# Kernel tuning notes

Hardware: AMD Instinct MI355X
Metric: run time of the kernel (lower is better)

Reference implementation:

```python
import jax, jax.numpy as jnp
import numpy as np

B = 8388608  # batch

def moth(x, a, b):
    # per-feature parametric elementwise activation: a * x * sigmoid(b * x)
    return a * x * jax.nn.sigmoid(b * x)

def setup_inputs() -> dict:
    key = jax.random.key(0)
    ks = jax.random.split(key, 12)
    inp = {
        'x':  jax.random.normal(ks[0], (B, 2), dtype=jnp.float32),
        'W1': jax.random.normal(ks[1], (2, 8), dtype=jnp.float32) * (1.0 / np.sqrt(2)),
        'b1': jax.random.normal(ks[2], (8,), dtype=jnp.float32) * 0.01,
        'a1': jax.random.normal(ks[3], (8,), dtype=jnp.float32) * 0.1 + 1.0,
        'c1': jax.random.normal(ks[4], (8,), dtype=jnp.float32) * 0.1 + 1.0,
        'W2': jax.random.normal(ks[5], (8, 4), dtype=jnp.float32) * (1.0 / np.sqrt(8)),
        'b2': jax.random.normal(ks[6], (4,), dtype=jnp.float32) * 0.01,
        'a2': jax.random.normal(ks[7], (4,), dtype=jnp.float32) * 0.1 + 1.0,
        'c2': jax.random.normal(ks[8], (4,), dtype=jnp.float32) * 0.1 + 1.0,
        'W3': jax.random.normal(ks[9], (4, 1), dtype=jnp.float32) * (1.0 / np.sqrt(4)),
        'b3': jax.random.normal(ks[10], (1,), dtype=jnp.float32) * 0.01,
    }
    return inp

def reference(x, W1, b1, a1, c1, W2, b2, a2, c2, W3, b3):
    h = x @ W1 + b1            # [B, 8]
    h = moth(h, a1, c1)        # [B, 8]
    h = h @ W2 + b2            # [B, 4]
    h = moth(h, a2, c2)        # [B, 4]
    out = h @ W3 + b3          # [B, 1]
    return out
```

## Files before the change

kernel.cpp:

```cpp
#include <hip/hip_runtime.h>

#define NLOG2E -1.44269504088896340736f

typedef float f32x2 __attribute__((ext_vector_type(2)));


__global__ void prefold_kernel(
    const float* __restrict__ W1, const float* __restrict__ b1,
    const float* __restrict__ a1, const float* __restrict__ c1,
    const float* __restrict__ W2, const float* __restrict__ b2,
    const float* __restrict__ a2, const float* __restrict__ c2,
    const float* __restrict__ W3, const float* __restrict__ b3,
    float* __restrict__ C)
{
    if (threadIdx.x == 0 && blockIdx.x == 0) {
        for (int j = 0; j < 8; ++j) {
            float ncl = c1[j] * NLOG2E;
            C[j]      = W1[j]     * ncl;
            C[8 + j]  = W1[8 + j] * ncl;
            C[16 + j] = b1[j]     * ncl;
            float k1 = a1[j] / ncl;
            for (int k = 0; k < 4; ++k)
                C[24 + j * 4 + k] = W2[j * 4 + k] * k1;
        }
        for (int k = 0; k < 4; ++k) {
            C[56 + k] = b2[k];
            C[60 + k] = c2[k] * NLOG2E;
            C[64 + k] = a2[k] * W3[k];
        }
        C[68] = b3[0];
    }
}

__device__ __forceinline__ f32x2 moth2(float4 p, const f32x2* __restrict__ Cp,
                                       float bb3)
{
    f32x2 u[2][4];
#pragma unroll
    for (int r = 0; r < 2; ++r) {
        float X0 = r ? p.z : p.x;
        float X1 = r ? p.w : p.y;
        f32x2 x0b = {X0, X0};
        f32x2 x1b = {X1, X1};
#pragma unroll
        for (int pj = 0; pj < 4; ++pj)
            u[r][pj] = __builtin_elementwise_fma(
                           x0b, Cp[pj],
                           __builtin_elementwise_fma(x1b, Cp[4 + pj],
                                                     Cp[8 + pj]));
    }

#pragma unroll
    for (int r = 0; r < 2; ++r)
#pragma unroll
        for (int pj = 0; pj < 4; ++pj) {
            f32x2 e;
            e[0] = __builtin_amdgcn_exp2f(u[r][pj][0]);
            e[1] = __builtin_amdgcn_exp2f(u[r][pj][1]);
            f32x2 d = e + 1.0f;
            f32x2 s;
            s[0] = __builtin_amdgcn_rcpf(d[0]);
            s[1] = __builtin_amdgcn_rcpf(d[1]);
            u[r][pj] *= s;
        }

    f32x2 res;
#pragma unroll
    for (int r = 0; r < 2; ++r) {
        f32x2 ta = Cp[28], tb = Cp[29];
#pragma unroll
        for (int j = 0; j < 8; ++j) {
            float hj = u[r][j >> 1][j & 1];
            f32x2 hb = {hj, hj};
            ta = __builtin_elementwise_fma(hb, Cp[12 + j * 2 + 0], ta);
            tb = __builtin_elementwise_fma(hb, Cp[12 + j * 2 + 1], tb);
        }
        f32x2 u2a = Cp[30] * ta;
        f32x2 u2b = Cp[31] * tb;
        f32x2 ea, eb;
        ea[0] = __builtin_amdgcn_exp2f(u2a[0]);
        ea[1] = __builtin_amdgcn_exp2f(u2a[1]);
        eb[0] = __builtin_amdgcn_exp2f(u2b[0]);
        eb[1] = __builtin_amdgcn_exp2f(u2b[1]);
        f32x2 da = ea + 1.0f, db = eb + 1.0f;
        f32x2 sa, sb;
        sa[0] = __builtin_amdgcn_rcpf(da[0]);
        sa[1] = __builtin_amdgcn_rcpf(da[1]);
        sb[0] = __builtin_amdgcn_rcpf(db[0]);
        sb[1] = __builtin_amdgcn_rcpf(db[1]);
        f32x2 pa = ta * sa;
        f32x2 pb = tb * sb;
        f32x2 acc = {bb3, 0.0f};
        acc = __builtin_elementwise_fma(pa, Cp[32], acc);
        acc = __builtin_elementwise_fma(pb, Cp[33], acc);
        res[r] = acc[0] + acc[1];
    }
    return res;
}

__global__ __launch_bounds__(256, 4) void PlaygroundModel_66365834658304_kernel(
    const float* __restrict__ x, const float* __restrict__ C,
    float* __restrict__ out, int rows)
{
    const f32x2* Cp = (const f32x2*)C;
    float bb3 = C[68];

    int g = blockIdx.x * blockDim.x + threadIdx.x;
    int lane = g & 63;
    long long idx0 = (long long)(g >> 6) * 256 + lane;
    long long n4f  = (long long)rows >> 1;

    const float4* x4 = (const float4*)x;
    f32x2* o2 = (f32x2*)out;

    if (idx0 + 192 < n4f) {
        float4 P0 = x4[idx0];
        float4 P1 = x4[idx0 + 64];
        float4 P2 = x4[idx0 + 128];
        float4 P3 = x4[idx0 + 192];
        o2[idx0]       = moth2(P0, Cp, bb3);
        o2[idx0 + 64]  = moth2(P1, Cp, bb3);
        o2[idx0 + 128] = moth2(P2, Cp, bb3);
        o2[idx0 + 192] = moth2(P3, Cp, bb3);
    } else {
        const float* uw0  = C;
        const float* uw1  = C + 8;
        const float* ub   = C + 16;
        const float* w2f  = C + 24;
        const float* bb2  = C + 56;
        const float* ncl2 = C + 60;
        const float* aw2  = C + 64;
#pragma unroll
        for (int k = 0; k < 4; ++k) {
            long long idx = idx0 + 64 * k;
            long long r0 = idx * 2;
            for (long long rr = r0; rr < r0 + 2 && rr < rows; ++rr) {
                float x0 = x[rr * 2 + 0], x1 = x[rr * 2 + 1];
                float h[8];
#pragma unroll
                for (int j = 0; j < 8; ++j) {
                    float uu = fmaf(x0, uw0[j], fmaf(x1, uw1[j], ub[j]));
                    float s  = __builtin_amdgcn_rcpf(
                                   1.0f + __builtin_amdgcn_exp2f(uu));
                    h[j] = uu * s;
                }
                float o = bb3;
#pragma unroll
                for (int kk = 0; kk < 4; ++kk) {
                    float t = bb2[kk];
#pragma unroll
                    for (int j = 0; j < 8; ++j)
                        t = fmaf(h[j], w2f[j * 4 + kk], t);
                    float u2 = ncl2[kk] * t;
                    float sg = __builtin_amdgcn_rcpf(
                                   1.0f + __builtin_amdgcn_exp2f(u2));
                    o = fmaf(t * sg, aw2[kk], o);
                }
                out[rr] = o;
            }
        }
    }
}

extern "C" void kernel_launch(void* const* d_in, const int* in_sizes, int n_in,
                              void* d_out, int out_size, void* d_ws, size_t ws_size,
                              hipStream_t stream) {
    const float* x  = (const float*)d_in[0];
    const float* W1 = (const float*)d_in[1];
    const float* b1 = (const float*)d_in[2];
    const float* a1 = (const float*)d_in[3];
    const float* c1 = (const float*)d_in[4];
    const float* W2 = (const float*)d_in[5];
    const float* b2 = (const float*)d_in[6];
    const float* a2 = (const float*)d_in[7];
    const float* c2 = (const float*)d_in[8];
    const float* W3 = (const float*)d_in[9];
    const float* b3 = (const float*)d_in[10];
    float* out = (float*)d_out;
    float* C   = (float*)d_ws;

    prefold_kernel<<<1, 64, 0, stream>>>(W1, b1, a1, c1, W2, b2, a2, c2,
                                         W3, b3, C);

    int rows = in_sizes[0] / 2;
    long long n4    = ((long long)rows + 1) / 2;
    long long waves = (n4 + 255) / 256;
    long long thr   = waves * 64;
    int block = 256;
    long long grid = (thr + block - 1) / block;
    if (grid < 1) grid = 1;

    PlaygroundModel_66365834658304_kernel<<<(int)grid, block, 0, stream>>>(
        x, C, out, rows);
}
```

Before: 127.1 us.

## Switch to grid-stride loop with software-prefetched loads and capped grid

```diff
diff --git a/kernel.cpp b/kernel.cpp
--- a/kernel.cpp
+++ b/kernel.cpp
@@ -98,31 +98,36 @@
     return res;
 }
 
-__global__ __launch_bounds__(256, 4) void PlaygroundModel_66365834658304_kernel(
+__global__ __launch_bounds__(256, 6) void PlaygroundModel_66365834658304_kernel(
     const float* __restrict__ x, const float* __restrict__ C,
     float* __restrict__ out, int rows)
 {
     const f32x2* Cp = (const f32x2*)C;
     float bb3 = C[68];
 
-    int g = blockIdx.x * blockDim.x + threadIdx.x;
-    int lane = g & 63;
-    long long idx0 = (long long)(g >> 6) * 256 + lane;
-    long long n4f  = (long long)rows >> 1;
+    long long n4f    = (long long)rows >> 1;
+    long long g      = (long long)blockIdx.x * blockDim.x + threadIdx.x;
+    long long stride = (long long)gridDim.x * blockDim.x;
 
     const float4* x4 = (const float4*)x;
     f32x2* o2 = (f32x2*)out;
 
-    if (idx0 + 192 < n4f) {
-        float4 P0 = x4[idx0];
-        float4 P1 = x4[idx0 + 64];
-        float4 P2 = x4[idx0 + 128];
-        float4 P3 = x4[idx0 + 192];
-        o2[idx0]       = moth2(P0, Cp, bb3);
-        o2[idx0 + 64]  = moth2(P1, Cp, bb3);
-        o2[idx0 + 128] = moth2(P2, Cp, bb3);
-        o2[idx0 + 192] = moth2(P3, Cp, bb3);
-    } else {
+    long long idx = g;
+    if (idx < n4f) {
+        float4 p = x4[idx];
+        for (;;) {
+            long long nidx = idx + stride;
+            bool has = (nidx < n4f);
+            float4 np;
+            if (has) np = x4[nidx];
+            o2[idx] = moth2(p, Cp, bb3);
+            if (!has) break;
+            p = np;
+            idx = nidx;
+        }
+    }
+
+    if (g == 0 && (rows & 1)) {
         const float* uw0  = C;
         const float* uw1  = C + 8;
         const float* ub   = C + 16;
@@ -130,35 +135,28 @@
         const float* bb2  = C + 56;
         const float* ncl2 = C + 60;
         const float* aw2  = C + 64;
+        long long rr = (long long)rows - 1;
+        float x0 = x[rr * 2 + 0], x1 = x[rr * 2 + 1];
+        float h[8];
 #pragma unroll
-        for (int k = 0; k < 4; ++k) {
-            long long idx = idx0 + 64 * k;
-            long long r0 = idx * 2;
-            for (long long rr = r0; rr < r0 + 2 && rr < rows; ++rr) {
-                float x0 = x[rr * 2 + 0], x1 = x[rr * 2 + 1];
-                float h[8];
+        for (int j = 0; j < 8; ++j) {
+            float uu = fmaf(x0, uw0[j], fmaf(x1, uw1[j], ub[j]));
+            float s  = __builtin_amdgcn_rcpf(
+                           1.0f + __builtin_amdgcn_exp2f(uu));
+            h[j] = uu * s;
+        }
+        float o = bb3;
 #pragma unroll
-                for (int j = 0; j < 8; ++j) {
-                    float uu = fmaf(x0, uw0[j], fmaf(x1, uw1[j], ub[j]));
-                    float s  = __builtin_amdgcn_rcpf(
-                                   1.0f + __builtin_amdgcn_exp2f(uu));
-                    h[j] = uu * s;
-                }
-                float o = bb3;
+        for (int kk = 0; kk < 4; ++kk) {
+            float t = bb2[kk];
 #pragma unroll
-                for (int kk = 0; kk < 4; ++kk) {
-                    float t = bb2[kk];
-#pragma unroll
-                    for (int j = 0; j < 8; ++j)
-                        t = fmaf(h[j], w2f[j * 4 + kk], t);
-                    float u2 = ncl2[kk] * t;
-                    float sg = __builtin_amdgcn_rcpf(
-                                   1.0f + __builtin_amdgcn_exp2f(u2));
-                    o = fmaf(t * sg, aw2[kk], o);
-                }
-                out[rr] = o;
-            }
+            for (int j = 0; j < 8; ++j) t = fmaf(h[j], w2f[j * 4 + kk], t);
+            float u2 = ncl2[kk] * t;
+            float sg = __builtin_amdgcn_rcpf(
+                           1.0f + __builtin_amdgcn_exp2f(u2));
+            o = fmaf(t * sg, aw2[kk], o);
         }
+        out[rr] = o;
     }
 }
 
@@ -183,13 +181,12 @@
                                          W3, b3, C);
 
     int rows = in_sizes[0] / 2;
-    long long n4    = ((long long)rows + 1) / 2;
-    long long waves = (n4 + 255) / 256;
-    long long thr   = waves * 64;
+    long long n4 = (long long)rows >> 1;
+
     int block = 256;
-    long long grid = (thr + block - 1) / block;
-    if (grid < 1) grid = 1;
+    long long want = (n4 + (long long)block * 4 - 1) / ((long long)block * 4);
+    int grid = (int)(want < 1 ? 1 : (want > 4096 ? 4096 : want));
 
-    PlaygroundModel_66365834658304_kernel<<<(int)grid, block, 0, stream>>>(
+    PlaygroundModel_66365834658304_kernel<<<grid, block, 0, stream>>>(
         x, C, out, rows);
 }
```

Measured after the change: 129.7 us. 2.1% more time.
